# Performance work log

Hardware: AMD Instinct MI355X
Metric: run time of the kernel (lower is better)

## Reference

```python
import jax, jax.numpy as jnp
import numpy as np

NUM_HEADS = 8
LN_EPS = 1e-5


def setup_inputs() -> dict:
    key = jax.random.key(0)
    ks = jax.random.split(key, 8)
    B, H, W, C = 2, 64, 64, 256
    return {
        "x": jax.random.normal(ks[0], (B, H, W, C), dtype=jnp.float32),
        "cond": jax.random.normal(ks[1], (B, C), dtype=jnp.float32),
        "t": jax.random.randint(ks[2], (B,), 0, 100, dtype=jnp.int64),
        "emb_table": jax.random.normal(ks[3], (100, C), dtype=jnp.float32) * 0.02,
        "ada_w": jax.random.normal(ks[4], (C, 2 * C), dtype=jnp.float32) * 0.02,
        "ada_b": jnp.zeros((2 * C,), dtype=jnp.float32),
        "qkv_w": jax.random.normal(ks[5], (C, 3 * C), dtype=jnp.float32) * 0.02,
        "qkv_b": jnp.zeros((3 * C,), dtype=jnp.float32),
        "proj_w": jax.random.normal(ks[6], (C, C), dtype=jnp.float32) * 0.02,
        "proj_b": jnp.zeros((C,), dtype=jnp.float32),
    }


def reference(x, cond, t, emb_table, ada_w, ada_b, qkv_w, qkv_b, proj_w, proj_b):
    B, H, W, C = x.shape
    N = H * W
    h = NUM_HEADS
    d = C // h
    scale = d ** -0.5

    x = x.reshape(B, N, C)

    # AdaLayerNorm (adalayernorm_abs): timestep embedding -> SiLU -> Linear -> scale/shift
    emb = emb_table[t]                                # [B, C]
    ss = jax.nn.silu(emb) @ ada_w + ada_b             # [B, 2C]
    sc, sh = jnp.split(ss, 2, axis=-1)                # each [B, C]
    mu = jnp.mean(x, axis=-1, keepdims=True)
    var = jnp.var(x, axis=-1, keepdims=True)
    xn = (x - mu) * jax.lax.rsqrt(var + LN_EPS)       # LN without affine
    x = xn * (1.0 + sc[:, None, :]) + sh[:, None, :]

    # QKV projection and head split
    qkv = (x @ qkv_w + qkv_b).reshape(B, N, 3, h, d)
    qkv = jnp.transpose(qkv, (2, 0, 3, 1, 4))          # [3, B, h, N, d]
    q, k, v = qkv[0], qkv[1], qkv[2]

    # Manual attention: full [B, h, N, N] scores (matches original module)
    attn = jnp.einsum('bhnd,bhmd->bhnm', q, k) * scale
    attn = jax.nn.softmax(attn, axis=-1)
    out = jnp.einsum('bhnm,bhmd->bhnd', attn, v)       # [B, h, N, d]
    out = jnp.transpose(out, (0, 2, 1, 3)).reshape(B, N, C)

    out = (out.reshape(B, H, W, C) @ proj_w) + proj_b
    return out
```

## Files before the change

kernel.cpp:

```cpp
#include <hip/hip_runtime.h>
#include <hip/hip_bf16.h>
#include <stdint.h>

typedef __attribute__((ext_vector_type(8))) short bfrag;
typedef __attribute__((ext_vector_type(4))) short bfrag4;
typedef __attribute__((ext_vector_type(4))) float f32x4;
typedef __attribute__((ext_vector_type(2))) float f32x2;
typedef __attribute__((ext_vector_type(2))) unsigned int u32x2;

__device__ inline short f2bf(float f) {
  union { float f; uint32_t u; } v; v.f = f;
  uint32_t u = v.u;
  uint32_t r = (u + 0x7fffu + ((u >> 16) & 1u)) >> 16;
  return (short)r;
}

__device__ inline uint32_t pack_bf16(float a, float b) {
  uint32_t ua = __builtin_bit_cast(uint32_t, a) + 0x8000u;
  uint32_t ub = __builtin_bit_cast(uint32_t, b) + 0x8000u;
  return __builtin_amdgcn_perm(ub, ua, 0x07060302);
}

__global__ __launch_bounds__(256) void ada_kernel(
    const float* __restrict__ emb_table, const int* __restrict__ t,
    const float* __restrict__ ada_w, const float* __restrict__ ada_b,
    float* __restrict__ scsh) {
  int b = blockIdx.y;
  int tid = threadIdx.x;
  __shared__ float se[256];
  __shared__ float part[256];
  int tt = t[b];
  float e = emb_table[tt * 256 + tid];
  se[tid] = e / (1.f + __expf(-e));
  __syncthreads();
  int ol = tid & 63, kc = tid >> 6;
  int o = blockIdx.x * 64 + ol;
  float acc = 0.f;
#pragma unroll 8
  for (int k = kc * 64; k < (kc + 1) * 64; ++k) acc += se[k] * ada_w[k * 512 + o];
  part[tid] = acc;
  __syncthreads();
  if (tid < 64) {
    int oo = blockIdx.x * 64 + tid;
    scsh[b * 512 + oo] =
        part[tid] + part[64 + tid] + part[128 + tid] + part[192 + tid] + ada_b[oo];
  }
}

__global__ __launch_bounds__(256) void transpose_w(const float* __restrict__ W,
                                                   short* __restrict__ Wt, int N) {
  __shared__ float tile[64][65];
  int k0 = blockIdx.x * 64, n0 = blockIdx.y * 64;
  int tid = threadIdx.x;
  int r = tid >> 2, c0 = (tid & 3) * 16;
  const float* src = W + (long)(k0 + r) * N + n0 + c0;
#pragma unroll
  for (int j = 0; j < 16; j += 4) {
    float4 v = *(const float4*)(src + j);
    tile[r][c0 + j] = v.x; tile[r][c0 + j + 1] = v.y;
    tile[r][c0 + j + 2] = v.z; tile[r][c0 + j + 3] = v.w;
  }
  __syncthreads();
  int nl = tid >> 2, kc = (tid & 3) * 16;
  short outv[16];
#pragma unroll
  for (int j = 0; j < 16; ++j) outv[j] = f2bf(tile[kc + j][nl]);
  short* dst = Wt + (long)(n0 + nl) * 256 + k0 + kc;
  *(bfrag*)dst = *(bfrag*)&outv[0];
  *(bfrag*)(dst + 8) = *(bfrag*)&outv[8];
}

__global__ __launch_bounds__(256) void ln_kernel(const float* __restrict__ x,
                                                 const float* __restrict__ scsh,
                                                 short* __restrict__ xb) {
  int row = blockIdx.x;
  int b = row >> 12;
  int i = threadIdx.x;
  float v = x[(long)row * 256 + i];
  float s = v, sq = v * v;
#pragma unroll
  for (int off = 32; off > 0; off >>= 1) {
    s += __shfl_down(s, off);
    sq += __shfl_down(sq, off);
  }
  __shared__ float red[8];
  int w = i >> 6;
  if ((i & 63) == 0) { red[w] = s; red[4 + w] = sq; }
  __syncthreads();
  s = red[0] + red[1] + red[2] + red[3];
  sq = red[4] + red[5] + red[6] + red[7];
  float mu = s * (1.f / 256.f);
  float var = sq * (1.f / 256.f) - mu * mu;
  float xn = (v - mu) * rsqrtf(var + 1e-5f);
  float y = xn * (1.f + scsh[b * 512 + i]) + scsh[b * 512 + 256 + i];
  xb[(long)row * 256 + i] = f2bf(y);
}

__global__ __launch_bounds__(256) void gemm_bf16(const short* __restrict__ A,
                                                 const short* __restrict__ Bt,
                                                 const float* __restrict__ bias,
                                                 int N, int mode, float qscale,
                                                 short* __restrict__ qk,
                                                 short* __restrict__ vT,
                                                 float* __restrict__ cout) {
  __shared__ short As[64 * 40];
  __shared__ short Bs[64 * 40];
  const int mt = blockIdx.x, nt = blockIdx.y;
  const int tid = threadIdx.x;
  const int w = tid >> 6, lane = tid & 63, l16 = lane & 15, quad = lane >> 4;
  const int si = tid >> 2, sk = (tid & 3) * 8;
  f32x4 acc[4] = {{0,0,0,0},{0,0,0,0},{0,0,0,0},{0,0,0,0}};
  const short* Arow = A + (long)(mt * 64 + si) * 256 + sk;
  const short* Brow = Bt + (long)(nt * 64 + si) * 256 + sk;
  for (int kk = 0; kk < 8; ++kk) {
    __syncthreads();
    *(bfrag*)&As[si * 40 + sk] = *(const bfrag*)(Arow + kk * 32);
    *(bfrag*)&Bs[si * 40 + sk] = *(const bfrag*)(Brow + kk * 32);
    __syncthreads();
    bfrag a = *(const bfrag*)&As[(w * 16 + l16) * 40 + quad * 8];
#pragma unroll
    for (int c = 0; c < 4; ++c) {
      bfrag bf = *(const bfrag*)&Bs[(c * 16 + l16) * 40 + quad * 8];
      acc[c] = __builtin_amdgcn_mfma_f32_16x16x32_bf16(a, bf, acc[c], 0, 0, 0);
    }
  }
  const int row0 = mt * 64 + w * 16 + quad * 4;
  if (mode == 1) {
#pragma unroll
    for (int c = 0; c < 4; ++c) {
      int col = nt * 64 + c * 16 + l16;
      float bv = bias[col];
#pragma unroll
      for (int r = 0; r < 4; ++r)
        cout[(long)(row0 + r) * N + col] = acc[c][r] + bv;
    }
  } else if (nt < 8) {
#pragma unroll
    for (int c = 0; c < 4; ++c) {
      int col = nt * 64 + c * 16 + l16;
      float bv = bias[col];
      float mult = (col < 256) ? qscale : 1.0f;
#pragma unroll
      for (int r = 0; r < 4; ++r)
        qk[(long)(row0 + r) * 512 + col] = f2bf((acc[c][r] + bv) * mult);
    }
  } else {
    const int bb = mt >> 6;
    const int keyl = row0 & 4095;
#pragma unroll
    for (int c = 0; c < 4; ++c) {
      int col = nt * 64 + c * 16 + l16;
      float bv = bias[col];
      int d = col - 512;
      u32x2 dd;
      dd.x = pack_bf16(acc[c][0] + bv, acc[c][1] + bv);
      dd.y = pack_bf16(acc[c][2] + bv, acc[c][3] + bv);
      *(u32x2*)&vT[((long)(bb * 8 + (d >> 5)) * 32 + (d & 31)) * 4096 + keyl] = dd;
    }
  }
}

__global__ __launch_bounds__(256) void attn_kernel(const short* __restrict__ qk,
                                                   const short* __restrict__ vT,
                                                   short* __restrict__ attn_out) {
  const int blk = blockIdx.x;
  const int qt = blk & 31;
  const int bh = blk >> 5;
  const int b = bh >> 3, hh = bh & 7;
  const int tid = threadIdx.x;
  const int w = tid >> 6, lane = tid & 63, l16 = lane & 15, quad = lane >> 4;

  __shared__ short Ks[2][64 * 40];
  __shared__ short Vt[2][32 * 68];

  const long rowbase = (long)b * 4096;
  const int qrow0 = qt * 128 + w * 32 + l16;
  bfrag qf0 = *(const bfrag*)&qk[(rowbase + qrow0) * 512 + hh * 32 + quad * 8];
  bfrag qf1 = *(const bfrag*)&qk[(rowbase + qrow0 + 16) * 512 + hh * 32 + quad * 8];

  f32x4 o00 = {0,0,0,0}, o10 = {0,0,0,0};
  f32x4 o01 = {0,0,0,0}, o11 = {0,0,0,0};
  f32x2 l0 = {0.f, 0.f}, l1 = {0.f, 0.f};

  const int si = tid >> 2, sk = (tid & 3) * 8;
  const int vrow = tid >> 3, vcol = (tid & 7) * 8;
  const short* ksrc = qk + rowbase * 512 + 256 + hh * 32 + (long)si * 512 + sk;
  const short* vsrc = vT + ((long)bh * 32 + vrow) * 4096 + vcol;

  bfrag k8 = *(const bfrag*)ksrc;
  bfrag v8 = *(const bfrag*)vsrc;

  int buf = 0;
  for (int kt = 0; kt < 64; ++kt) {
    *(bfrag*)&Ks[buf][si * 40 + sk] = k8;
    *(bfrag*)&Vt[buf][vrow * 68 + vcol] = v8;
    int ktn = (kt < 63) ? (kt + 1) : 63;
    k8 = *(const bfrag*)(ksrc + (long)ktn * 64 * 512);
    v8 = *(const bfrag*)(vsrc + ktn * 64);
    __syncthreads();

    f32x4 s0[4], s1[4];
#pragma unroll
    for (int nt = 0; nt < 4; ++nt) {
      bfrag kf = *(const bfrag*)&Ks[buf][(nt * 16 + l16) * 40 + quad * 8];
      f32x4 z = {0,0,0,0};
      s0[nt] = __builtin_amdgcn_mfma_f32_16x16x32_bf16(kf, qf0, z, 0, 0, 0);
      s1[nt] = __builtin_amdgcn_mfma_f32_16x16x32_bf16(kf, qf1, z, 0, 0, 0);
    }
    bfrag4 pb0[4], pb1[4];
#pragma unroll
    for (int nt = 0; nt < 4; ++nt) {
      float a0 = __builtin_amdgcn_exp2f(s0[nt][0]);
      float a1 = __builtin_amdgcn_exp2f(s0[nt][1]);
      float a2 = __builtin_amdgcn_exp2f(s0[nt][2]);
      float a3 = __builtin_amdgcn_exp2f(s0[nt][3]);
      f32x2 pa = {a0, a1}, pc = {a2, a3};
      l0 += pa; l0 += pc;
      u32x2 pk0; pk0.x = pack_bf16(a0, a1); pk0.y = pack_bf16(a2, a3);
      pb0[nt] = __builtin_bit_cast(bfrag4, pk0);
      float b0 = __builtin_amdgcn_exp2f(s1[nt][0]);
      float b1 = __builtin_amdgcn_exp2f(s1[nt][1]);
      float b2 = __builtin_amdgcn_exp2f(s1[nt][2]);
      float b3 = __builtin_amdgcn_exp2f(s1[nt][3]);
      f32x2 pb = {b0, b1}, pd = {b2, b3};
      l1 += pb; l1 += pd;
      u32x2 pk1; pk1.x = pack_bf16(b0, b1); pk1.y = pack_bf16(b2, b3);
      pb1[nt] = __builtin_bit_cast(bfrag4, pk1);
    }
#pragma unroll
    for (int nt = 0; nt < 4; ++nt) {
      bfrag4 va = *(const bfrag4*)&Vt[buf][l16 * 68 + nt * 16 + quad * 4];
      bfrag4 vb = *(const bfrag4*)&Vt[buf][(16 + l16) * 68 + nt * 16 + quad * 4];
      o00 = __builtin_amdgcn_mfma_f32_16x16x16bf16_1k(va, pb0[nt], o00, 0, 0, 0);
      o10 = __builtin_amdgcn_mfma_f32_16x16x16bf16_1k(vb, pb0[nt], o10, 0, 0, 0);
      o01 = __builtin_amdgcn_mfma_f32_16x16x16bf16_1k(va, pb1[nt], o01, 0, 0, 0);
      o11 = __builtin_amdgcn_mfma_f32_16x16x16bf16_1k(vb, pb1[nt], o11, 0, 0, 0);
    }
    buf ^= 1;
  }
  float ls0 = l0.x + l0.y, ls1 = l1.x + l1.y;
  ls0 += __shfl_xor(ls0, 16); ls0 += __shfl_xor(ls0, 32);
  ls1 += __shfl_xor(ls1, 16); ls1 += __shfl_xor(ls1, 32);
  float inv0 = 1.f / ls0, inv1 = 1.f / ls1;
  long ob0 = (rowbase + qrow0) * 256 + hh * 32;
  long ob1 = (rowbase + qrow0 + 16) * 256 + hh * 32;
#pragma unroll
  for (int h = 0; h < 2; ++h) {
    f32x4 g0 = h ? o10 : o00;
    f32x4 g1 = h ? o11 : o01;
#pragma unroll
    for (int r2 = 0; r2 < 2; ++r2) {
      *(uint32_t*)&attn_out[ob0 + h * 16 + quad * 4 + 2 * r2] =
          pack_bf16(g0[2 * r2] * inv0, g0[2 * r2 + 1] * inv0);
      *(uint32_t*)&attn_out[ob1 + h * 16 + quad * 4 + 2 * r2] =
          pack_bf16(g1[2 * r2] * inv1, g1[2 * r2 + 1] * inv1);
    }
  }
}

extern "C" void kernel_launch(void* const* d_in, const int* in_sizes, int n_in,
                              void* d_out, int out_size, void* d_ws, size_t ws_size,
                              hipStream_t stream) {
  const float* x      = (const float*)d_in[0];
  const int*   t      = (const int*)d_in[2];
  const float* emb    = (const float*)d_in[3];
  const float* ada_w  = (const float*)d_in[4];
  const float* ada_b  = (const float*)d_in[5];
  const float* qkv_w  = (const float*)d_in[6];
  const float* qkv_b  = (const float*)d_in[7];
  const float* proj_w = (const float*)d_in[8];
  const float* proj_b = (const float*)d_in[9];

  char* ws = (char*)d_ws;
  float* scsh     = (float*)(ws);
  short* qkv_wt   = (short*)(ws + 4096);
  short* proj_wt  = (short*)(ws + 397312);
  short* xb       = (short*)(ws + 528384);
  short* qk_out   = (short*)(ws + 4722688);
  short* vT       = (short*)(ws + 13111296);
  short* attn_out = (short*)(ws + 17305600);

  const float QS = 0.17677669529663687f * 1.4426950408889634f;

  ada_kernel<<<dim3(8, 2), 256, 0, stream>>>(emb, t, ada_w, ada_b, scsh);
  transpose_w<<<dim3(4, 12), 256, 0, stream>>>(qkv_w, qkv_wt, 768);
  transpose_w<<<dim3(4, 4), 256, 0, stream>>>(proj_w, proj_wt, 256);
  ln_kernel<<<8192, 256, 0, stream>>>(x, scsh, xb);
  gemm_bf16<<<dim3(128, 12), 256, 0, stream>>>(xb, qkv_wt, qkv_b, 768, 0, QS,
                                               qk_out, vT, nullptr);
  attn_kernel<<<512, 256, 0, stream>>>(qk_out, vT, attn_out);
  gemm_bf16<<<dim3(128, 4), 256, 0, stream>>>(attn_out, proj_wt, proj_b, 256, 1,
                                              1.0f, nullptr, nullptr, (float*)d_out);
}
```

Measured before the change: 182.4 us.

## Split attention over two key halves and reduce partials in a separate kernel

The attention kernel now splits the key range into two halves, launching twice as many blocks. Each block writes unnormalized fp32 partial outputs and row sums to workspace, and a new reduce kernel sums the halves, normalizes and writes bf16. The aim is better occupancy and latency hiding on a 256-CU part, since 512 blocks gave only about two per CU. The cost is an extra kernel launch and roughly 34 MB of fp32 partial traffic. The bf16 packing also switches to the hardware cvt_pk_bf16_f32 builtin when it is available.

```diff
diff --git a/kernel.cpp b/kernel.cpp
--- a/kernel.cpp
+++ b/kernel.cpp
@@ -15,11 +15,19 @@
   return (short)r;
 }
 
+#if __has_builtin(__builtin_amdgcn_cvt_pk_bf16_f32)
+typedef __attribute__((ext_vector_type(2))) __bf16 bf16x2_t;
+__device__ inline uint32_t pack_bf16(float a, float b) {
+  bf16x2_t r = __builtin_amdgcn_cvt_pk_bf16_f32(a, b);
+  return __builtin_bit_cast(uint32_t, r);
+}
+#else
 __device__ inline uint32_t pack_bf16(float a, float b) {
   uint32_t ua = __builtin_bit_cast(uint32_t, a) + 0x8000u;
   uint32_t ub = __builtin_bit_cast(uint32_t, b) + 0x8000u;
   return __builtin_amdgcn_perm(ub, ua, 0x07060302);
 }
+#endif
 
 __global__ __launch_bounds__(256) void ada_kernel(
     const float* __restrict__ emb_table, const int* __restrict__ t,
@@ -162,10 +170,12 @@
 
 __global__ __launch_bounds__(256) void attn_kernel(const short* __restrict__ qk,
                                                    const short* __restrict__ vT,
-                                                   short* __restrict__ attn_out) {
+                                                   float* __restrict__ Opart,
+                                                   float* __restrict__ lpart) {
   const int blk = blockIdx.x;
   const int qt = blk & 31;
-  const int bh = blk >> 5;
+  const int bh = (blk >> 5) & 15;
+  const int ks = blk >> 9;
   const int b = bh >> 3, hh = bh & 7;
   const int tid = threadIdx.x;
   const int w = tid >> 6, lane = tid & 63, l16 = lane & 15, quad = lane >> 4;
@@ -187,16 +197,17 @@
   const short* ksrc = qk + rowbase * 512 + 256 + hh * 32 + (long)si * 512 + sk;
   const short* vsrc = vT + ((long)bh * 32 + vrow) * 4096 + vcol;
 
-  bfrag k8 = *(const bfrag*)ksrc;
-  bfrag v8 = *(const bfrag*)vsrc;
+  const int kt0 = ks * 32;
+  bfrag k8 = *(const bfrag*)(ksrc + (long)kt0 * 64 * 512);
+  bfrag v8 = *(const bfrag*)(vsrc + kt0 * 64);
 
   int buf = 0;
-  for (int kt = 0; kt < 64; ++kt) {
+  for (int i = 0; i < 32; ++i) {
     *(bfrag*)&Ks[buf][si * 40 + sk] = k8;
     *(bfrag*)&Vt[buf][vrow * 68 + vcol] = v8;
-    int ktn = (kt < 63) ? (kt + 1) : 63;
-    k8 = *(const bfrag*)(ksrc + (long)ktn * 64 * 512);
-    v8 = *(const bfrag*)(vsrc + ktn * 64);
+    int nn = (i < 31) ? (i + 1) : 31;
+    k8 = *(const bfrag*)(ksrc + (long)(kt0 + nn) * 64 * 512);
+    v8 = *(const bfrag*)(vsrc + (kt0 + nn) * 64);
     __syncthreads();
 
     f32x4 s0[4], s1[4];
@@ -241,21 +252,32 @@
   float ls0 = l0.x + l0.y, ls1 = l1.x + l1.y;
   ls0 += __shfl_xor(ls0, 16); ls0 += __shfl_xor(ls0, 32);
   ls1 += __shfl_xor(ls1, 16); ls1 += __shfl_xor(ls1, 32);
-  float inv0 = 1.f / ls0, inv1 = 1.f / ls1;
-  long ob0 = (rowbase + qrow0) * 256 + hh * 32;
-  long ob1 = (rowbase + qrow0 + 16) * 256 + hh * 32;
-#pragma unroll
-  for (int h = 0; h < 2; ++h) {
-    f32x4 g0 = h ? o10 : o00;
-    f32x4 g1 = h ? o11 : o01;
-#pragma unroll
-    for (int r2 = 0; r2 < 2; ++r2) {
-      *(uint32_t*)&attn_out[ob0 + h * 16 + quad * 4 + 2 * r2] =
-          pack_bf16(g0[2 * r2] * inv0, g0[2 * r2 + 1] * inv0);
-      *(uint32_t*)&attn_out[ob1 + h * 16 + quad * 4 + 2 * r2] =
-          pack_bf16(g1[2 * r2] * inv1, g1[2 * r2 + 1] * inv1);
-    }
-  }
+  const long pbase0 = (((long)ks * 16 + bh) * 4096 + qrow0) * 32;
+  const long pbase1 = pbase0 + 16 * 32;
+  *(f32x4*)&Opart[pbase0 + quad * 4] = o00;
+  *(f32x4*)&Opart[pbase0 + 16 + quad * 4] = o10;
+  *(f32x4*)&Opart[pbase1 + quad * 4] = o01;
+  *(f32x4*)&Opart[pbase1 + 16 + quad * 4] = o11;
+  if (quad == 0) {
+    lpart[((long)ks * 16 + bh) * 4096 + qrow0] = ls0;
+    lpart[((long)ks * 16 + bh) * 4096 + qrow0 + 16] = ls1;
+  }
+}
+
+__global__ __launch_bounds__(256) void reduce_kernel(const float* __restrict__ Opart,
+                                                     const float* __restrict__ lpart,
+                                                     short* __restrict__ attn_out) {
+  int row = blockIdx.x;
+  int bq = row >> 12, q = row & 4095;
+  int d = threadIdx.x;
+  int h2 = d >> 5, dd = d & 31;
+  int bh = bq * 8 + h2;
+  long i0 = (((long)bh) * 4096 + q) * 32 + dd;
+  long i1 = i0 + (long)16 * 4096 * 32;
+  float l0 = lpart[(long)bh * 4096 + q];
+  float l1 = lpart[(long)(16 + bh) * 4096 + q];
+  float val = (Opart[i0] + Opart[i1]) / (l0 + l1);
+  attn_out[(long)row * 256 + d] = f2bf(val);
 }
 
 extern "C" void kernel_launch(void* const* d_in, const int* in_sizes, int n_in,
@@ -279,6 +301,8 @@
   short* qk_out   = (short*)(ws + 4722688);
   short* vT       = (short*)(ws + 13111296);
   short* attn_out = (short*)(ws + 17305600);
+  float* Opart    = (float*)(ws + 21499904);
+  float* lpart    = (float*)(ws + 38277120);
 
   const float QS = 0.17677669529663687f * 1.4426950408889634f;
 
@@ -288,7 +312,8 @@
   ln_kernel<<<8192, 256, 0, stream>>>(x, scsh, xb);
   gemm_bf16<<<dim3(128, 12), 256, 0, stream>>>(xb, qkv_wt, qkv_b, 768, 0, QS,
                                                qk_out, vT, nullptr);
-  attn_kernel<<<512, 256, 0, stream>>>(qk_out, vT, attn_out);
+  attn_kernel<<<1024, 256, 0, stream>>>(qk_out, vT, Opart, lpart);
+  reduce_kernel<<<8192, 256, 0, stream>>>(Opart, lpart, attn_out);
   gemm_bf16<<<dim3(128, 4), 256, 0, stream>>>(attn_out, proj_wt, proj_b, 256, 1,
                                               1.0f, nullptr, nullptr, (float*)d_out);
 }
```

New measurement: 182.9 us. Within noise of the previous version (+0.3%).
